# Performance work log

Hardware: AMD Instinct MI355X
Metric: run time of the kernel (lower is better)

The kernel has to match this reference:

```python
import jax, jax.numpy as jnp
import numpy as np

CENTER_VAR = 0.1
SIZE_VAR = 0.2
SCORE_THR = 0.01
NMS_THR = 0.45
PRE_NMS = 200   # per-class candidates kept before NMS
MAX_DET = 100   # final detections per image


def setup_inputs() -> dict:
    key = jax.random.key(0)
    k1, k2, k3, k4 = jax.random.split(key, 4)
    B, N, C = 32, 24564, 81
    cls_logits = jax.random.normal(k1, (B, N, C), jnp.float32)
    bbox_pred = jax.random.normal(k2, (B, N, 4), jnp.float32)
    # priors in center form (cx, cy, w, h), normalized coords
    cxy = jax.random.uniform(k3, (N, 2), jnp.float32)
    wh = jax.random.uniform(k4, (N, 2), jnp.float32, 0.02, 0.3)
    priors = jnp.concatenate([cxy, wh], axis=-1)
    return {"cls_logits": cls_logits, "bbox_pred": bbox_pred, "priors": priors}


def decode_boxes(loc, priors):
    # convert_locations_to_boxes + center_form_to_corner_form, fused
    cxy = loc[..., :2] * CENTER_VAR * priors[..., 2:] + priors[..., :2]
    wh = jnp.exp(loc[..., 2:] * SIZE_VAR) * priors[..., 2:]
    return jnp.concatenate([cxy - wh * 0.5, cxy + wh * 0.5], axis=-1)  # [..., 4] corners


def iou_matrix(boxes):  # boxes [P,4] corner form -> [P,P]
    lt = jnp.maximum(boxes[:, None, :2], boxes[None, :, :2])
    rb = jnp.minimum(boxes[:, None, 2:], boxes[None, :, 2:])
    inter = jnp.prod(jnp.clip(rb - lt, 0.0), axis=-1)
    area = jnp.prod(jnp.clip(boxes[:, 2:] - boxes[:, :2], 0.0), axis=-1)
    union = area[:, None] + area[None, :] - inter
    return inter / jnp.maximum(union, 1e-9)


def nms_one_class(scores, boxes):
    # scores [N], boxes [N,4]; returns post-NMS scores [PRE_NMS], boxes [PRE_NMS,4]
    sc, idx = jax.lax.top_k(jnp.where(scores > SCORE_THR, scores, 0.0), PRE_NMS)
    bx = boxes[idx]                       # [P,4], sorted by score desc
    iou = iou_matrix(bx)                  # [P,P]
    valid = sc > 0.0

    def body(supp, i):
        keep_i = valid[i] & ~supp[i]
        supp = supp | (keep_i & (iou[i] > NMS_THR))
        return supp, keep_i

    _, keep = jax.lax.scan(body, jnp.zeros(PRE_NMS, bool), jnp.arange(PRE_NMS))
    return sc * keep.astype(sc.dtype), bx


def reference(cls_logits, bbox_pred, priors):
    B, N, C = cls_logits.shape
    scores = jax.nn.softmax(cls_logits, axis=-1)       # [B,N,C]
    boxes = decode_boxes(bbox_pred, priors)            # [B,N,4]
    fg = scores[..., 1:]                               # drop background, [B,N,C-1]

    per_image = jax.vmap(nms_one_class, in_axes=(0, None))  # over classes
    cls_sc, cls_bx = jax.vmap(lambda s, b: per_image(jnp.swapaxes(s, 0, 1), b))(fg, boxes)
    # cls_sc [B,C-1,P], cls_bx [B,C-1,P,4]

    flat_sc = cls_sc.reshape(B, -1)                    # [B,(C-1)*P]
    det_sc, fidx = jax.lax.top_k(flat_sc, MAX_DET)     # [B,MAX_DET]
    flat_bx = cls_bx.reshape(B, -1, 4)
    det_bx = jnp.take_along_axis(flat_bx, fidx[..., None], axis=1)  # [B,MAX_DET,4]
    det_lb = (fidx // PRE_NMS + 1).astype(jnp.int32)   # 1-based class labels
    return det_bx, det_sc, det_lb
```

## Files before the change

kernel.cpp:

```cpp
#include <hip/hip_runtime.h>
#include <cstdint>

#define B_IMG 32
#define N_PRI 24564
#define N_CLS 81
#define N_FG  80
#define PRE   200
#define MAXD  100
#define NBINS 1024
#define CANDS 512
#define SNAP_ULPS 2
#define SMX_ROWS 16

#define SCORE_THR_F 0.01f
#define NMS_THR_D   0.45
#define CENTER_VAR_D 0.1
#define SIZE_VAR_D   0.2

__global__ void decode_kernel(const float* __restrict__ bbox,
                              const float* __restrict__ priors,
                              double* __restrict__ boxes) {
  int n = blockIdx.x * blockDim.x + threadIdx.x;
  int b = blockIdx.y;
  if (n >= N_PRI) return;
  float4 loc = ((const float4*)bbox)[(size_t)b * N_PRI + n];
  float4 pr  = ((const float4*)priors)[n];
  double cx = ((double)loc.x * CENTER_VAR_D) * (double)pr.z + (double)pr.x;
  double cy = ((double)loc.y * CENTER_VAR_D) * (double)pr.w + (double)pr.y;
  double w  = exp((double)loc.z * SIZE_VAR_D) * (double)pr.z;
  double h  = exp((double)loc.w * SIZE_VAR_D) * (double)pr.w;
  double* o = boxes + ((size_t)b * N_PRI + n) * 4;
  double2 lo, hi;
  lo.x = cx - w * 0.5; lo.y = cy - h * 0.5;
  hi.x = cx + w * 0.5; hi.y = cy + h * 0.5;
  ((double2*)o)[0] = lo;
  ((double2*)o)[1] = hi;
}

__device__ __forceinline__ double fexp(double y) {
  const double LOG2E = 1.4426950408889634074;
  const double LN2HI = 6.93147180369123816490e-01;
  const double LN2LO = 1.90821492927058770002e-10;
  double kd = rint(y * LOG2E);
  int k = (int)kd;
  if (k < -1020) return 0.0;
  double r = fma(-kd, LN2HI, y);
  r = fma(-kd, LN2LO, r);
  double p =             2.7557319223985891e-06;
  p = fma(p, r, 2.4801587301587302e-05);
  p = fma(p, r, 1.9841269841269841e-04);
  p = fma(p, r, 1.3888888888888889e-03);
  p = fma(p, r, 8.3333333333333332e-03);
  p = fma(p, r, 4.1666666666666664e-02);
  p = fma(p, r, 1.6666666666666666e-01);
  p = fma(p, r, 0.5);
  p = fma(p, r, 1.0);
  p = fma(p, r, 1.0);
  double s = __longlong_as_double(((long long)(k + 1023)) << 52);
  return p * s;
}

__global__ __launch_bounds__(64, 4) void softmax_fg_kernel(
    const float* __restrict__ logits, float* __restrict__ fgT, int b0) {
  __shared__ float F[N_FG * SMX_ROWS];
  int t = threadIdx.x;
  int j = t & 3;
  int r = t >> 2;
  int lb = blockIdx.y;
  int b  = b0 + lb;
  int n  = blockIdx.x * SMX_ROWS + r;
  bool act = (n < N_PRI);

  float lv[21];
  float m = -__builtin_huge_valf();
  if (act) {
    const float* row = logits + ((size_t)b * N_PRI + n) * N_CLS;
#pragma unroll
    for (int k = 0; k < 21; ++k) {
      int c = j + 4 * k;
      if (c < N_CLS) { lv[k] = row[c]; m = fmaxf(m, lv[k]); }
    }
  }
  m = fmaxf(m, __shfl_xor(m, 1, 64));
  m = fmaxf(m, __shfl_xor(m, 2, 64));
  double dm = (double)m;

  double ev[21];
  double s0 = 0.0, s1 = 0.0;
  if (act) {
#pragma unroll
    for (int k = 0; k < 21; ++k) {
      int c = j + 4 * k;
      if (c < N_CLS) {
        ev[k] = fexp((double)lv[k] - dm);
        if (k & 1) s1 += ev[k]; else s0 += ev[k];
      }
    }
  }
  double s = s0 + s1;
  s += __shfl_xor(s, 1, 64);
  s += __shfl_xor(s, 2, 64);
  double inv = 1.0 / s;

  unsigned pu[21];
  unsigned long long mlo = 0ull, mhi = 0ull;
  int jm1 = j - 1;
  if (act) {
#pragma unroll
    for (int k = 0; k < 21; ++k) {
      int c = j + 4 * k;
      if (c >= 1 && c < N_CLS) {
        float p = (float)(ev[k] * inv);
        float pv = (p > SCORE_THR_F) ? p : 0.0f;
        F[(c - 1) * SMX_ROWS + r] = pv;
        pu[k] = __float_as_uint(pv);
        if (pu[k] != 0u) {
          int f = 4 * k + jm1;
          if (f < 64) mlo |= 1ull << f;
          else        mhi |= 1ull << (f - 64);
        }
      } else pu[k] = 0u;
    }
  }
  mlo |= __shfl_xor(mlo, 1, 64);
  mlo |= __shfl_xor(mlo, 2, 64);
  mhi |= __shfl_xor(mhi, 1, 64);
  mhi |= __shfl_xor(mhi, 2, 64);

  if (act) {
    unsigned long long mask  = mlo & ~1ull;
    unsigned long long maskh = mhi;
    int c2 = -1;
    if (mask)       { c2 = __ffsll(mask) - 1;       mask  &= mask - 1; }
    else if (maskh) { c2 = 64 + __ffsll(maskh) - 1; maskh &= maskh - 1; }
    float v2 = (c2 >= 0) ? F[c2 * SMX_ROWS + r] : 0.0f;
    while (c2 >= 0) {
      int c2n = -1;
      if (mask)       { c2n = __ffsll(mask) - 1;       mask  &= mask - 1; }
      else if (maskh) { c2n = 64 + __ffsll(maskh) - 1; maskh &= maskh - 1; }
      float vnext = (c2n >= 0) ? F[c2n * SMX_ROWS + r] : 0.0f;

      unsigned u2m = __float_as_uint(v2) - 2u;
      int found = 255;
#pragma unroll
      for (int k = 0; k < 21; ++k) {
        unsigned du = pu[k] - u2m;
        int cls = 4 * k + jm1;
        if (du <= 4u) found = min(found, cls);
      }
      found = min(found, __shfl_xor(found, 1, 64));
      found = min(found, __shfl_xor(found, 2, 64));
      if (found < c2) {
        float vf = F[found * SMX_ROWS + r];
        if (j == 0) F[c2 * SMX_ROWS + r] = vf;
        int kk = (c2 + 1) >> 2;
        if (((c2 + 1) & 3) == j) {
          unsigned nb = __float_as_uint(vf);
#pragma unroll
          for (int k = 0; k < 21; ++k) if (k == kk) pu[k] = nb;
        }
      }
      c2 = c2n; v2 = vnext;
    }
  }

  if (act) {
    float* outb = fgT + (size_t)lb * N_FG * N_PRI + n;
#pragma unroll
    for (int k = 0; k < 21; ++k) {
      int c = j + 4 * k;
      if (c >= 1 && c < N_CLS)
        outb[(size_t)(c - 1) * N_PRI] = __uint_as_float(pu[k]);
    }
  }
}

__global__ __launch_bounds__(256) void topk_kernel(const float* __restrict__ fgT,
                                                   float* __restrict__ topk_sc,
                                                   int* __restrict__ topk_idx, int b0) {
  __shared__ unsigned int hist[NBINS];
  __shared__ unsigned long long cand[CANDS];
  __shared__ unsigned int part[256];
  __shared__ int s_cut;
  __shared__ unsigned int s_cnt;
  int t = threadIdx.x;
  int c = blockIdx.x;
  int lb = blockIdx.y;
  int gb = b0 + lb;
  const float* src = fgT + ((size_t)lb * N_FG + c) * N_PRI;

  for (int i = t; i < NBINS; i += 256) hist[i] = 0;
  if (t == 0) s_cnt = 0;
  __syncthreads();

  for (int i = t; i < N_PRI; i += 256) {
    float v = src[i];
    if (v > 0.0f) atomicAdd(&hist[__float_as_uint(v) >> 21], 1u);
  }
  __syncthreads();

  unsigned s = 0;
  for (int j = 0; j < 4; ++j) s += hist[t * 4 + j];
  part[t] = s;
  __syncthreads();

  if (t == 0) {
    unsigned acc = 0; int cut = -1;
    for (int tb = 255; tb >= 0 && cut < 0; --tb) {
      unsigned pa = part[tb];
      if (acc + pa >= PRE) {
        for (int bin = tb * 4 + 3; bin >= tb * 4; --bin) {
          acc += hist[bin];
          if (acc >= PRE) { cut = bin; break; }
        }
      } else acc += pa;
    }
    s_cut = (cut < 0) ? 0 : cut;
  }
  __syncthreads();
  int cut = s_cut;

  for (int i = t; i < N_PRI; i += 256) {
    float v = src[i];
    if (v > 0.0f) {
      unsigned u = __float_as_uint(v);
      if ((int)(u >> 21) >= cut) {
        unsigned pos = atomicAdd(&s_cnt, 1u);
        if (pos < CANDS)
          cand[pos] = ((unsigned long long)u << 32) |
                      (unsigned long long)(0xFFFFFFFFu - (unsigned)i);
      }
    }
  }
  __syncthreads();
  unsigned cnt = s_cnt; if (cnt > CANDS) cnt = CANDS;
  for (int i = t; i < CANDS; i += 256)
    if ((unsigned)i >= cnt) cand[i] = 0ull;
  __syncthreads();

  for (int k = 2; k <= CANDS; k <<= 1) {
    for (int j = k >> 1; j > 0; j >>= 1) {
      for (int i = t; i < CANDS; i += 256) {
        int ixj = i ^ j;
        if (ixj > i) {
          unsigned long long a = cand[i], bb = cand[ixj];
          bool up = ((i & k) == 0);
          if (up ? (a < bb) : (a > bb)) { cand[i] = bb; cand[ixj] = a; }
        }
      }
      __syncthreads();
    }
  }

  if (t < PRE) {
    unsigned long long key = cand[t];
    float v = __uint_as_float((unsigned)(key >> 32));
    unsigned idx = 0xFFFFFFFFu - (unsigned)(key & 0xFFFFFFFFull);
    if (idx >= N_PRI) idx = 0;
    size_t o = ((size_t)gb * N_FG + c) * PRE + t;
    topk_sc[o] = v;
    topk_idx[o] = (int)idx;
  }
}

__global__ __launch_bounds__(64) void nms_kernel(const float* __restrict__ topk_sc,
                                                 const int* __restrict__ topk_idx,
                                                 const double* __restrict__ boxes,
                                                 float* __restrict__ cls_sc) {
  __shared__ double bx[PRE][4];
  __shared__ double ar[PRE];
  __shared__ float sc[PRE];
  __shared__ unsigned char supp[PRE];
  int t = threadIdx.x;
  int c = blockIdx.x, b = blockIdx.y;
  size_t base = ((size_t)b * N_FG + c) * PRE;

  for (int k = t; k < PRE; k += 64) {
    int idx = topk_idx[base + k];
    const double* bp = boxes + ((size_t)b * N_PRI + idx) * 4;
    double x1 = bp[0], y1 = bp[1], x2 = bp[2], y2 = bp[3];
    bx[k][0] = x1; bx[k][1] = y1; bx[k][2] = x2; bx[k][3] = y2;
    ar[k] = fmax(x2 - x1, 0.0) * fmax(y2 - y1, 0.0);
    sc[k] = topk_sc[base + k];
    supp[k] = 0;
  }
  __syncthreads();

  double mybx[4][4]; double mya[4]; bool mykeep[4];
  for (int r = 0; r < 4; ++r) {
    int k = t + r * 64;
    mykeep[r] = false;
    if (k < PRE) {
      mybx[r][0] = bx[k][0]; mybx[r][1] = bx[k][1];
      mybx[r][2] = bx[k][2]; mybx[r][3] = bx[k][3];
      mya[r] = ar[k];
    }
  }

  for (int i = 0; i < PRE; ++i) {
    bool keep_i = (sc[i] > 0.0f) && (supp[i] == 0);
    if ((i & 63) == t) mykeep[i >> 6] = keep_i;
    if (keep_i) {
      double x1 = bx[i][0], y1 = bx[i][1], x2 = bx[i][2], y2 = bx[i][3];
      double ai = ar[i];
      for (int r = 0; r < 4; ++r) {
        int k = t + r * 64;
        if (k < PRE && k > i) {
          double xx1 = fmax(x1, mybx[r][0]), yy1 = fmax(y1, mybx[r][1]);
          double xx2 = fmin(x2, mybx[r][2]), yy2 = fmin(y2, mybx[r][3]);
          double inter = fmax(xx2 - xx1, 0.0) * fmax(yy2 - yy1, 0.0);
          double uni = fmax(ai + mya[r] - inter, 1e-9);
          if (inter / uni > NMS_THR_D) supp[k] = 1;
        }
      }
    }
    __syncthreads();
  }

  for (int r = 0; r < 4; ++r) {
    int k = t + r * 64;
    if (k < PRE) cls_sc[base + k] = mykeep[r] ? sc[k] : 0.0f;
  }
}

__global__ __launch_bounds__(256) void final_kernel(const float* __restrict__ cls_sc,
                                                    const int* __restrict__ topk_idx,
                                                    const double* __restrict__ boxes,
                                                    float* __restrict__ out) {
  __shared__ unsigned int hist[NBINS];
  __shared__ unsigned long long cand[CANDS];
  __shared__ unsigned int part[256];
  __shared__ int s_cut;
  __shared__ unsigned int s_cnt;
  const int M = N_FG * PRE;
  int t = threadIdx.x, b = blockIdx.x;
  const float* src = cls_sc + (size_t)b * M;

  for (int i = t; i < NBINS; i += 256) hist[i] = 0;
  if (t == 0) s_cnt = 0;
  __syncthreads();

  for (int i = t; i < M; i += 256) {
    float v = src[i];
    if (v > 0.0f) atomicAdd(&hist[__float_as_uint(v) >> 21], 1u);
  }
  __syncthreads();

  unsigned s = 0;
  for (int j = 0; j < 4; ++j) s += hist[t * 4 + j];
  part[t] = s;
  __syncthreads();

  if (t == 0) {
    unsigned acc = 0; int cut = -1;
    for (int tb = 255; tb >= 0 && cut < 0; --tb) {
      unsigned pa = part[tb];
      if (acc + pa >= MAXD) {
        for (int bin = tb * 4 + 3; bin >= tb * 4; --bin) {
          acc += hist[bin];
          if (acc >= MAXD) { cut = bin; break; }
        }
      } else acc += pa;
    }
    s_cut = (cut < 0) ? 0 : cut;
  }
  __syncthreads();
  int cut = s_cut;

  for (int i = t; i < M; i += 256) {
    float v = src[i];
    if (v > 0.0f) {
      unsigned u = __float_as_uint(v);
      if ((int)(u >> 21) >= cut) {
        unsigned pos = atomicAdd(&s_cnt, 1u);
        if (pos < CANDS)
          cand[pos] = ((unsigned long long)u << 32) |
                      (unsigned long long)(0xFFFFFFFFu - (unsigned)i);
      }
    }
  }
  __syncthreads();
  unsigned cnt = s_cnt; if (cnt > CANDS) cnt = CANDS;
  for (int i = t; i < CANDS; i += 256)
    if ((unsigned)i >= cnt) cand[i] = 0ull;
  __syncthreads();

  for (int k = 2; k <= CANDS; k <<= 1) {
    for (int j = k >> 1; j > 0; j >>= 1) {
      for (int i = t; i < CANDS; i += 256) {
        int ixj = i ^ j;
        if (ixj > i) {
          unsigned long long a = cand[i], bb = cand[ixj];
          bool up = ((i & k) == 0);
          if (up ? (a < bb) : (a > bb)) { cand[i] = bb; cand[ixj] = a; }
        }
      }
      __syncthreads();
    }
  }

  if (t < MAXD) {
    unsigned long long key = cand[t];
    float v = __uint_as_float((unsigned)(key >> 32));
    unsigned f = 0xFFFFFFFFu - (unsigned)(key & 0xFFFFFFFFull);
    if (f >= (unsigned)M) f = 0;
    int c = (int)(f / PRE), k = (int)(f % PRE);
    int idx = topk_idx[((size_t)b * N_FG + c) * PRE + k];
    if (idx < 0 || idx >= N_PRI) idx = 0;
    const double* bp = boxes + ((size_t)b * N_PRI + idx) * 4;
    float4 bb = make_float4((float)bp[0], (float)bp[1], (float)bp[2], (float)bp[3]);
    ((float4*)out)[b * MAXD + t] = bb;
    out[B_IMG * MAXD * 4 + b * MAXD + t] = v;
    out[B_IMG * MAXD * 5 + b * MAXD + t] = (float)(c + 1);
  }
}

extern "C" void kernel_launch(void* const* d_in, const int* in_sizes, int n_in,
                              void* d_out, int out_size, void* d_ws, size_t ws_size,
                              hipStream_t stream) {
  const float* cls_logits = (const float*)d_in[0];
  const float* bbox_pred  = (const float*)d_in[1];
  const float* priors     = (const float*)d_in[2];
  float* out = (float*)d_out;

  double* boxes   = (double*)d_ws;
  float* topk_sc  = (float*)(boxes + (size_t)B_IMG * N_PRI * 4);
  int*   topk_idx = (int*)(topk_sc + (size_t)B_IMG * N_FG * PRE);
  float* cls_sc   = (float*)(topk_idx + (size_t)B_IMG * N_FG * PRE);
  float* fgT      = cls_sc + (size_t)B_IMG * N_FG * PRE;

  size_t persist_bytes = (size_t)((char*)fgT - (char*)d_ws);
  size_t per_b = (size_t)N_FG * N_PRI * sizeof(float);
  int chunkB = 1;
  if (ws_size > persist_bytes) {
    size_t cb = (ws_size - persist_bytes) / per_b;
    chunkB = (cb >= (size_t)B_IMG) ? B_IMG : (cb < 1 ? 1 : (int)cb);
  }

  decode_kernel<<<dim3((N_PRI + 255) / 256, B_IMG), 256, 0, stream>>>(
      bbox_pred, priors, boxes);

  for (int b0 = 0; b0 < B_IMG; b0 += chunkB) {
    int nb = (B_IMG - b0) < chunkB ? (B_IMG - b0) : chunkB;
    softmax_fg_kernel<<<dim3((N_PRI + SMX_ROWS - 1) / SMX_ROWS, nb), 64, 0, stream>>>(
        cls_logits, fgT, b0);
    topk_kernel<<<dim3(N_FG, nb), 256, 0, stream>>>(
        fgT, topk_sc, topk_idx, b0);
  }

  nms_kernel<<<dim3(N_FG, B_IMG), 64, 0, stream>>>(
      topk_sc, topk_idx, boxes, cls_sc);

  final_kernel<<<B_IMG, 256, 0, stream>>>(
      cls_sc, topk_idx, boxes, out);
}
```

Measured before the change: 1.221 ms.

## Vectorize top-k scans, privatize histograms per wave, use DPP reductions and custom exp

The top-k and final selection kernels now read scores as float4 and map each element back to its flat index. The top-k histogram is split into one copy per wavefront to reduce LDS atomic contention. The softmax kernel swaps its shuffle-based min reduction for DPP moves and lowers its launch-bounds occupancy hint from 4 to 2. The decode kernel uses a simplified polynomial exp in place of the library exp, with single-constant ln2 reduction and no underflow guard, which could change results slightly for extreme inputs.

```diff
diff --git a/kernel.cpp b/kernel.cpp
--- a/kernel.cpp
+++ b/kernel.cpp
@@ -17,6 +17,33 @@
 #define CENTER_VAR_D 0.1
 #define SIZE_VAR_D   0.2
 
+__device__ __forceinline__ double fexp(double y) {
+  const double LOG2E = 1.4426950408889634074;
+  const double LN2   = 0.69314718055994530942;
+  double kd = rint(y * LOG2E);
+  double r = fma(-kd, LN2, y);
+  double p =             2.7557319223985891e-06;
+  p = fma(p, r, 2.4801587301587302e-05);
+  p = fma(p, r, 1.9841269841269841e-04);
+  p = fma(p, r, 1.3888888888888889e-03);
+  p = fma(p, r, 8.3333333333333332e-03);
+  p = fma(p, r, 4.1666666666666664e-02);
+  p = fma(p, r, 1.6666666666666666e-01);
+  p = fma(p, r, 0.5);
+  p = fma(p, r, 1.0);
+  p = fma(p, r, 1.0);
+  int k = (int)kd;
+  double s = __longlong_as_double(((long long)(k + 1023)) << 52);
+  return p * s;
+}
+
+__device__ __forceinline__ int qmin4(int x) {
+  int y = __builtin_amdgcn_mov_dpp(x, 0xB1, 0xf, 0xf, true);
+  x = min(x, y);
+  y = __builtin_amdgcn_mov_dpp(x, 0x4E, 0xf, 0xf, true);
+  return min(x, y);
+}
+
 __global__ void decode_kernel(const float* __restrict__ bbox,
                               const float* __restrict__ priors,
                               double* __restrict__ boxes) {
@@ -27,8 +54,8 @@
   float4 pr  = ((const float4*)priors)[n];
   double cx = ((double)loc.x * CENTER_VAR_D) * (double)pr.z + (double)pr.x;
   double cy = ((double)loc.y * CENTER_VAR_D) * (double)pr.w + (double)pr.y;
-  double w  = exp((double)loc.z * SIZE_VAR_D) * (double)pr.z;
-  double h  = exp((double)loc.w * SIZE_VAR_D) * (double)pr.w;
+  double w  = fexp((double)loc.z * SIZE_VAR_D) * (double)pr.z;
+  double h  = fexp((double)loc.w * SIZE_VAR_D) * (double)pr.w;
   double* o = boxes + ((size_t)b * N_PRI + n) * 4;
   double2 lo, hi;
   lo.x = cx - w * 0.5; lo.y = cy - h * 0.5;
@@ -37,30 +64,7 @@
   ((double2*)o)[1] = hi;
 }
 
-__device__ __forceinline__ double fexp(double y) {
-  const double LOG2E = 1.4426950408889634074;
-  const double LN2HI = 6.93147180369123816490e-01;
-  const double LN2LO = 1.90821492927058770002e-10;
-  double kd = rint(y * LOG2E);
-  int k = (int)kd;
-  if (k < -1020) return 0.0;
-  double r = fma(-kd, LN2HI, y);
-  r = fma(-kd, LN2LO, r);
-  double p =             2.7557319223985891e-06;
-  p = fma(p, r, 2.4801587301587302e-05);
-  p = fma(p, r, 1.9841269841269841e-04);
-  p = fma(p, r, 1.3888888888888889e-03);
-  p = fma(p, r, 8.3333333333333332e-03);
-  p = fma(p, r, 4.1666666666666664e-02);
-  p = fma(p, r, 1.6666666666666666e-01);
-  p = fma(p, r, 0.5);
-  p = fma(p, r, 1.0);
-  p = fma(p, r, 1.0);
-  double s = __longlong_as_double(((long long)(k + 1023)) << 52);
-  return p * s;
-}
-
-__global__ __launch_bounds__(64, 4) void softmax_fg_kernel(
+__global__ __launch_bounds__(64, 2) void softmax_fg_kernel(
     const float* __restrict__ logits, float* __restrict__ fgT, int b0) {
   __shared__ float F[N_FG * SMX_ROWS];
   int t = threadIdx.x;
@@ -148,8 +152,7 @@
         int cls = 4 * k + jm1;
         if (du <= 4u) found = min(found, cls);
       }
-      found = min(found, __shfl_xor(found, 1, 64));
-      found = min(found, __shfl_xor(found, 2, 64));
+      found = qmin4(found);
       if (found < c2) {
         float vf = F[found * SMX_ROWS + r];
         if (j == 0) F[c2 * SMX_ROWS + r] = vf;
@@ -178,29 +181,38 @@
 __global__ __launch_bounds__(256) void topk_kernel(const float* __restrict__ fgT,
                                                    float* __restrict__ topk_sc,
                                                    int* __restrict__ topk_idx, int b0) {
-  __shared__ unsigned int hist[NBINS];
+  __shared__ unsigned int hist[4][NBINS];
   __shared__ unsigned long long cand[CANDS];
   __shared__ unsigned int part[256];
   __shared__ int s_cut;
   __shared__ unsigned int s_cnt;
   int t = threadIdx.x;
+  int w = t >> 6;
   int c = blockIdx.x;
   int lb = blockIdx.y;
   int gb = b0 + lb;
   const float* src = fgT + ((size_t)lb * N_FG + c) * N_PRI;
-
-  for (int i = t; i < NBINS; i += 256) hist[i] = 0;
+  const float4* src4 = (const float4*)src;
+
+  unsigned int* hf = &hist[0][0];
+  for (int i = t; i < 4 * NBINS; i += 256) hf[i] = 0;
   if (t == 0) s_cnt = 0;
   __syncthreads();
 
-  for (int i = t; i < N_PRI; i += 256) {
-    float v = src[i];
-    if (v > 0.0f) atomicAdd(&hist[__float_as_uint(v) >> 21], 1u);
+  for (int i = t; i < N_PRI / 4; i += 256) {
+    float4 v = src4[i];
+    if (v.x > 0.0f) atomicAdd(&hist[w][__float_as_uint(v.x) >> 21], 1u);
+    if (v.y > 0.0f) atomicAdd(&hist[w][__float_as_uint(v.y) >> 21], 1u);
+    if (v.z > 0.0f) atomicAdd(&hist[w][__float_as_uint(v.z) >> 21], 1u);
+    if (v.w > 0.0f) atomicAdd(&hist[w][__float_as_uint(v.w) >> 21], 1u);
   }
   __syncthreads();
 
   unsigned s = 0;
-  for (int j = 0; j < 4; ++j) s += hist[t * 4 + j];
+  for (int jj = 0; jj < 4; ++jj) {
+    int bin = t * 4 + jj;
+    s += hist[0][bin] + hist[1][bin] + hist[2][bin] + hist[3][bin];
+  }
   part[t] = s;
   __syncthreads();
 
@@ -210,7 +222,7 @@
       unsigned pa = part[tb];
       if (acc + pa >= PRE) {
         for (int bin = tb * 4 + 3; bin >= tb * 4; --bin) {
-          acc += hist[bin];
+          acc += hist[0][bin] + hist[1][bin] + hist[2][bin] + hist[3][bin];
           if (acc >= PRE) { cut = bin; break; }
         }
       } else acc += pa;
@@ -220,15 +232,19 @@
   __syncthreads();
   int cut = s_cut;
 
-  for (int i = t; i < N_PRI; i += 256) {
-    float v = src[i];
-    if (v > 0.0f) {
-      unsigned u = __float_as_uint(v);
-      if ((int)(u >> 21) >= cut) {
-        unsigned pos = atomicAdd(&s_cnt, 1u);
-        if (pos < CANDS)
-          cand[pos] = ((unsigned long long)u << 32) |
-                      (unsigned long long)(0xFFFFFFFFu - (unsigned)i);
+  for (int i = t; i < N_PRI / 4; i += 256) {
+    float4 v = src4[i];
+    float vv[4] = {v.x, v.y, v.z, v.w};
+#pragma unroll
+    for (int e = 0; e < 4; ++e) {
+      if (vv[e] > 0.0f) {
+        unsigned u = __float_as_uint(vv[e]);
+        if ((int)(u >> 21) >= cut) {
+          unsigned pos = atomicAdd(&s_cnt, 1u);
+          if (pos < CANDS)
+            cand[pos] = ((unsigned long long)u << 32) |
+                        (unsigned long long)(0xFFFFFFFFu - (unsigned)(4 * i + e));
+        }
       }
     }
   }
@@ -239,9 +255,9 @@
   __syncthreads();
 
   for (int k = 2; k <= CANDS; k <<= 1) {
-    for (int j = k >> 1; j > 0; j >>= 1) {
+    for (int jj = k >> 1; jj > 0; jj >>= 1) {
       for (int i = t; i < CANDS; i += 256) {
-        int ixj = i ^ j;
+        int ixj = i ^ jj;
         if (ixj > i) {
           unsigned long long a = cand[i], bb = cand[ixj];
           bool up = ((i & k) == 0);
@@ -335,19 +351,23 @@
   const int M = N_FG * PRE;
   int t = threadIdx.x, b = blockIdx.x;
   const float* src = cls_sc + (size_t)b * M;
+  const float4* src4 = (const float4*)src;
 
   for (int i = t; i < NBINS; i += 256) hist[i] = 0;
   if (t == 0) s_cnt = 0;
   __syncthreads();
 
-  for (int i = t; i < M; i += 256) {
-    float v = src[i];
-    if (v > 0.0f) atomicAdd(&hist[__float_as_uint(v) >> 21], 1u);
+  for (int i = t; i < M / 4; i += 256) {
+    float4 v = src4[i];
+    if (v.x > 0.0f) atomicAdd(&hist[__float_as_uint(v.x) >> 21], 1u);
+    if (v.y > 0.0f) atomicAdd(&hist[__float_as_uint(v.y) >> 21], 1u);
+    if (v.z > 0.0f) atomicAdd(&hist[__float_as_uint(v.z) >> 21], 1u);
+    if (v.w > 0.0f) atomicAdd(&hist[__float_as_uint(v.w) >> 21], 1u);
   }
   __syncthreads();
 
   unsigned s = 0;
-  for (int j = 0; j < 4; ++j) s += hist[t * 4 + j];
+  for (int jj = 0; jj < 4; ++jj) s += hist[t * 4 + jj];
   part[t] = s;
   __syncthreads();
 
@@ -367,15 +387,19 @@
   __syncthreads();
   int cut = s_cut;
 
-  for (int i = t; i < M; i += 256) {
-    float v = src[i];
-    if (v > 0.0f) {
-      unsigned u = __float_as_uint(v);
-      if ((int)(u >> 21) >= cut) {
-        unsigned pos = atomicAdd(&s_cnt, 1u);
-        if (pos < CANDS)
-          cand[pos] = ((unsigned long long)u << 32) |
-                      (unsigned long long)(0xFFFFFFFFu - (unsigned)i);
+  for (int i = t; i < M / 4; i += 256) {
+    float4 v = src4[i];
+    float vv[4] = {v.x, v.y, v.z, v.w};
+#pragma unroll
+    for (int e = 0; e < 4; ++e) {
+      if (vv[e] > 0.0f) {
+        unsigned u = __float_as_uint(vv[e]);
+        if ((int)(u >> 21) >= cut) {
+          unsigned pos = atomicAdd(&s_cnt, 1u);
+          if (pos < CANDS)
+            cand[pos] = ((unsigned long long)u << 32) |
+                        (unsigned long long)(0xFFFFFFFFu - (unsigned)(4 * i + e));
+        }
       }
     }
   }
@@ -386,9 +410,9 @@
   __syncthreads();
 
   for (int k = 2; k <= CANDS; k <<= 1) {
-    for (int j = k >> 1; j > 0; j >>= 1) {
+    for (int jj = k >> 1; jj > 0; jj >>= 1) {
       for (int i = t; i < CANDS; i += 256) {
-        int ixj = i ^ j;
+        int ixj = i ^ jj;
         if (ixj > i) {
           unsigned long long a = cand[i], bb = cand[ixj];
           bool up = ((i & k) == 0);
```

Result: faster. 1.098 ms (-10.0%).
